# Kernel tuning notes

Hardware: AMD Instinct MI355X
Metric: run time of the kernel (lower is better)

The kernel has to match this reference:

```python
import jax, jax.numpy as jnp
import numpy as np

N = 50000
E = 800000
IN_C = 128
HID = 16
HEADS = 8
OUT_C = 16
NEG_SLOPE = 0.2


def setup_inputs() -> dict:
    key = jax.random.key(0)
    ks = jax.random.split(key, 10)
    s = 1.0 / np.sqrt(IN_C)
    s2 = 1.0 / np.sqrt(HID * HEADS)
    return {
        "x": jax.random.normal(ks[0], (N, IN_C), jnp.float32),
        "edge_index": jax.random.randint(ks[1], (2, E), 0, N, jnp.int64),
        "W1": jax.random.normal(ks[2], (IN_C, HEADS * HID), jnp.float32) * s,
        "a_src1": jax.random.normal(ks[3], (HEADS, HID), jnp.float32) * s,
        "a_dst1": jax.random.normal(ks[4], (HEADS, HID), jnp.float32) * s,
        "b1": jnp.zeros((HEADS * HID,), jnp.float32),
        "W2": jax.random.normal(ks[5], (HEADS * HID, OUT_C), jnp.float32) * s2,
        "a_src2": jax.random.normal(ks[6], (1, OUT_C), jnp.float32) * s2,
        "a_dst2": jax.random.normal(ks[7], (1, OUT_C), jnp.float32) * s2,
        "b2": jnp.zeros((OUT_C,), jnp.float32),
    }


def gat_layer(x, src, dst, W, a_src, a_dst):
    # x: [N, F_in]; W: [F_in, H*C]; a_src/a_dst: [H, C]
    H, C = a_src.shape
    h = (x @ W).reshape(N, H, C)                       # [N, H, C]
    al_s = jnp.einsum('nhc,hc->nh', h, a_src)          # [N, H]
    al_d = jnp.einsum('nhc,hc->nh', h, a_dst)
    e = jax.nn.leaky_relu(al_s[src] + al_d[dst], NEG_SLOPE)  # [E', H]
    # scatter-softmax over incoming edges of each target node
    m = jax.ops.segment_max(e, dst, num_segments=N)    # [N, H]
    w = jnp.exp(e - m[dst])                            # [E', H]
    denom = jax.ops.segment_sum(w, dst, num_segments=N)
    alpha = w / denom[dst]                             # [E', H]
    out = jax.ops.segment_sum(h[src] * alpha[:, :, None], dst, num_segments=N)
    return out                                         # [N, H, C]


def reference(x, edge_index, W1, a_src1, a_dst1, b1, W2, a_src2, a_dst2, b2):
    loops = jnp.arange(N, dtype=edge_index.dtype)
    src = jnp.concatenate([edge_index[0], loops])
    dst = jnp.concatenate([edge_index[1], loops])
    # layer 1: heads=8, concat=True
    h1 = gat_layer(x, src, dst, W1, a_src1, a_dst1).reshape(N, -1) + b1
    h1 = jax.nn.elu(h1)
    # layer 2: heads=1, concat=False (single head -> mean is identity)
    h2 = gat_layer(h1, src, dst, W2, a_src2, a_dst2)[:, 0, :] + b2
    return h2
```

## Files before the change

kernel.cpp:

```cpp
#include <hip/hip_runtime.h>
#include <hip/hip_fp16.h>
#include <math.h>

#define N_NODES 50000
#define NE      800000
#define INC     128
#define F1      128
#define HEADS   8
#define HID     16
#define OUTC    16
#define NEG     0.2f
#define NBKT    196
#define NPART   128
#define N1BLK   ((N_NODES + 63) / 64)

union H4 { ushort4 u; __half h[4]; };
union H8 { uint4 u; __half h[8]; };

typedef _Float16 f16x8 __attribute__((ext_vector_type(8)));
typedef float    f32x4 __attribute__((ext_vector_type(4)));

__global__ __launch_bounds__(256) void prep_kernel(const int* __restrict__ ei,
                                                   int* __restrict__ cnt,
                                                   const float* __restrict__ W1,
                                                   const float* __restrict__ as1,
                                                   const float* __restrict__ ad1,
                                                   __half* __restrict__ W1t,
                                                   __half* __restrict__ waT) {
    __shared__ int h[NBKT];
    int b = blockIdx.x, tid = threadIdx.x;
    if (b < NPART) {
        for (int i = tid; i < NBKT; i += 256) h[i] = 0;
        __syncthreads();
        for (int e = b * 256 + tid; e < NE; e += NPART * 256)
            atomicAdd(&h[ei[NE + e] >> 8], 1);
        __syncthreads();
        for (int i = tid; i < NBKT; i += 256) cnt[i * NPART + b] = h[i];
    } else if (b < NPART + 64) {
        int i = (b - NPART) * 256 + tid;
        int k = i >> 7, nn = i & 127;
        W1t[nn * 128 + k] = __float2half(W1[k * 128 + nn]);
    } else {
        int i = (b - NPART - 64) * 256 + tid;
        int col = i & 15, k = i >> 4;
        int hh = col & 7;
        const float* av = (col < 8) ? as1 : ad1;
        float s = 0.f;
        #pragma unroll
        for (int cc = 0; cc < 16; ++cc)
            s += W1[k * 128 + hh * 16 + cc] * av[hh * 16 + cc];
        waT[col * 128 + k] = __float2half(s);
    }
}

__global__ __launch_bounds__(1024) void scan25k(int* __restrict__ cnt) {
    __shared__ int part[1024];
    const int TOT = NBKT * NPART;
    const int PER = (TOT + 1023) / 1024;
    int tid = threadIdx.x;
    int base = tid * PER;
    int s = 0;
    for (int i = 0; i < PER; ++i) {
        int idx = base + i;
        if (idx < TOT) s += cnt[idx];
    }
    part[tid] = s; __syncthreads();
    for (int off = 1; off < 1024; off <<= 1) {
        int t = (tid >= off) ? part[tid - off] : 0;
        __syncthreads();
        part[tid] += t;
        __syncthreads();
    }
    int run = part[tid] - s;
    for (int i = 0; i < PER; ++i) {
        int idx = base + i;
        if (idx < TOT) { int v = cnt[idx]; cnt[idx] = run; run += v; }
    }
}

__global__ __launch_bounds__(256) void scatter_node1_kernel(
    const int* __restrict__ ei, const int* __restrict__ cnt, int* __restrict__ tmp,
    const float* __restrict__ x, const __half* __restrict__ W1t,
    const __half* __restrict__ waT,
    __half* __restrict__ hfeat, float* __restrict__ als, float* __restrict__ ald)
{
    __shared__ _Float16 Xh[64 * 136];
    __shared__ _Float16 Wt[128 * 136];
    int b = blockIdx.x, tid = threadIdx.x;

    if (b < NPART) {
        int* cur = (int*)Xh;
        for (int i = tid; i < NBKT; i += 256) cur[i] = cnt[i * NPART + b];
        __syncthreads();
        for (int e = b * 256 + tid; e < NE; e += NPART * 256) {
            int s = ei[e], d = ei[NE + e];
            int p = atomicAdd(&cur[d >> 8], 1);
            tmp[p] = s | ((d & 255) << 16);
        }
        return;
    }

    int n0 = (b - NPART) * 64;

    for (int idx = tid; idx < 128 * 16; idx += 256) {
        int row = idx >> 4, c8 = (idx & 15) * 8;
        *(uint4*)(&Wt[row * 136 + c8]) = ((const uint4*)W1t)[idx];
    }
    for (int idx = tid; idx < 64 * 32; idx += 256) {
        int m = idx >> 5, f4 = idx & 31;
        int n = n0 + m;
        float4 v = (n < N_NODES) ? ((const float4*)(x + (size_t)n * INC))[f4]
                                 : make_float4(0.f, 0.f, 0.f, 0.f);
        union { unsigned long long u; _Float16 h[4]; } p;
        p.h[0] = (_Float16)v.x; p.h[1] = (_Float16)v.y;
        p.h[2] = (_Float16)v.z; p.h[3] = (_Float16)v.w;
        *(unsigned long long*)(&Xh[m * 136 + f4 * 4]) = p.u;
    }
    __syncthreads();

    int wave = tid >> 6, lane = tid & 63;
    int colL = lane & 15, q = lane >> 4;
    int nb = wave * 32;

    f32x4 acc[4][2];
    #pragma unroll
    for (int mt = 0; mt < 4; ++mt)
        #pragma unroll
        for (int nt = 0; nt < 2; ++nt)
            acc[mt][nt] = (f32x4){0.f, 0.f, 0.f, 0.f};
    f32x4 acc2 = (f32x4){0.f, 0.f, 0.f, 0.f};

    #pragma unroll
    for (int kb = 0; kb < 4; ++kb) {
        int ko = kb * 32 + q * 8;
        f16x8 b0 = *(const f16x8*)(&Wt[(nb +  0 + colL) * 136 + ko]);
        f16x8 b1 = *(const f16x8*)(&Wt[(nb + 16 + colL) * 136 + ko]);
        #pragma unroll
        for (int mt = 0; mt < 4; ++mt) {
            f16x8 a = *(const f16x8*)(&Xh[(mt * 16 + colL) * 136 + ko]);
            acc[mt][0] = __builtin_amdgcn_mfma_f32_16x16x32_f16(a, b0, acc[mt][0], 0, 0, 0);
            acc[mt][1] = __builtin_amdgcn_mfma_f32_16x16x32_f16(a, b1, acc[mt][1], 0, 0, 0);
        }
        f16x8 bw = *(const f16x8*)(waT + colL * 128 + ko);
        f16x8 aw = *(const f16x8*)(&Xh[(wave * 16 + colL) * 136 + ko]);
        acc2 = __builtin_amdgcn_mfma_f32_16x16x32_f16(aw, bw, acc2, 0, 0, 0);
    }

    #pragma unroll
    for (int nt = 0; nt < 2; ++nt) {
        int col = nb + nt * 16 + colL;
        #pragma unroll
        for (int mt = 0; mt < 4; ++mt) {
            f32x4 d = acc[mt][nt];
            #pragma unroll
            for (int r = 0; r < 4; ++r) {
                int node = n0 + mt * 16 + q * 4 + r;
                if (node < N_NODES) hfeat[(size_t)node * F1 + col] = __float2half(d[r]);
            }
        }
    }
    #pragma unroll
    for (int r = 0; r < 4; ++r) {
        int node = n0 + wave * 16 + q * 4 + r;
        if (node < N_NODES) {
            if (colL < 8) als[node * 8 + colL] = acc2[r];
            else          ald[node * 8 + (colL - 8)] = acc2[r];
        }
    }
}

__global__ __launch_bounds__(256) void bucket_sort(const int* __restrict__ tmp,
                                                   const int* __restrict__ cnt,
                                                   int* __restrict__ rowstart,
                                                   int* __restrict__ csr) {
    __shared__ int h[256];
    int b = blockIdx.x, tid = threadIdx.x;
    int base = cnt[b * NPART];
    int end  = (b == NBKT - 1) ? NE : cnt[(b + 1) * NPART];
    h[tid] = 0; __syncthreads();
    for (int i = base + tid; i < end; i += 256)
        atomicAdd(&h[(tmp[i] >> 16) & 255], 1);
    __syncthreads();
    int v = h[tid];
    for (int off = 1; off < 256; off <<= 1) {
        int t = (tid >= off) ? h[tid - off] : 0;
        __syncthreads();
        h[tid] += t;
        __syncthreads();
    }
    int excl = h[tid] - v;
    int n = (b << 8) + tid;
    if (n <= N_NODES) rowstart[n] = base + excl;
    __syncthreads();
    h[tid] = excl;
    __syncthreads();
    for (int i = base + tid; i < end; i += 256) {
        int e = tmp[i];
        int p = base + atomicAdd(&h[(e >> 16) & 255], 1);
        csr[p] = e & 0xFFFF;
    }
}

__global__ __launch_bounds__(256) void agg1_kernel(
    const int* __restrict__ rowstart, const int* __restrict__ csr,
    const __half* __restrict__ h1, const float* __restrict__ als,
    const float* __restrict__ ald, const float* __restrict__ b1,
    __half* __restrict__ hout)
{
    int tid = threadIdx.x;
    int n = blockIdx.x * 16 + (tid >> 4);
    int lane = tid & 15;
    int c = lane * 8;
    int head = lane >> 1;
    float aldn = ald[n * 8 + head];
    float v0 = als[n * 8 + head] + aldn;
    v0 = fmaxf(v0, NEG * v0);
    float w0 = __expf(v0);
    float sum = w0;
    float a[8];
    {
        H8 hs; hs.u = *(const uint4*)(h1 + (size_t)n * F1 + c);
        #pragma unroll
        for (int i = 0; i < 8; ++i) a[i] = w0 * __half2float(hs.h[i]);
    }
    int r0 = rowstart[n], r1 = rowstart[n + 1];

    float vA = 0.f, vB = 0.f;
    H8 hA, hB; hA.u = make_uint4(0,0,0,0); hB.u = hA.u;
    int sC = 0, sD = 0;
    if (r0 < r1) {
        int s = csr[r0];
        float t = als[s * 8 + head] + aldn;
        vA = fmaxf(t, NEG * t);
        hA.u = *(const uint4*)(h1 + (size_t)s * F1 + c);
    }
    if (r0 + 1 < r1) {
        int s = csr[r0 + 1];
        float t = als[s * 8 + head] + aldn;
        vB = fmaxf(t, NEG * t);
        hB.u = *(const uint4*)(h1 + (size_t)s * F1 + c);
    }
    if (r0 + 2 < r1) sC = csr[r0 + 2];
    if (r0 + 3 < r1) sD = csr[r0 + 3];

    int k = r0;
    for (; k + 1 < r1; k += 2) {
        float vcA = vA, vcB = vB;
        H8 hcA = hA, hcB = hB;
        int sE = (k + 4 < r1) ? csr[k + 4] : 0;
        int sF = (k + 5 < r1) ? csr[k + 5] : 0;
        if (k + 2 < r1) {
            float t = als[sC * 8 + head] + aldn;
            vA = fmaxf(t, NEG * t);
            hA.u = *(const uint4*)(h1 + (size_t)sC * F1 + c);
        }
        if (k + 3 < r1) {
            float t = als[sD * 8 + head] + aldn;
            vB = fmaxf(t, NEG * t);
            hB.u = *(const uint4*)(h1 + (size_t)sD * F1 + c);
        }
        sC = sE; sD = sF;
        float wA = __expf(vcA), wB = __expf(vcB);
        sum += wA + wB;
        #pragma unroll
        for (int i = 0; i < 8; ++i) {
            a[i] = fmaf(wA, __half2float(hcA.h[i]), a[i]);
            a[i] = fmaf(wB, __half2float(hcB.h[i]), a[i]);
        }
    }
    if (k < r1) {
        float wA = __expf(vA);
        sum += wA;
        #pragma unroll
        for (int i = 0; i < 8; ++i) a[i] = fmaf(wA, __half2float(hA.h[i]), a[i]);
    }

    float inv = 1.0f / sum;
    H8 t;
    #pragma unroll
    for (int i = 0; i < 8; ++i) {
        float o = a[i] * inv + b1[c + i];
        o = o > 0.f ? o : (__expf(o) - 1.0f);
        t.h[i] = __float2half(o);
    }
    *(uint4*)(hout + (size_t)n * F1 + c) = t.u;
}

__global__ __launch_bounds__(256) void node2_kernel(
    const __half* __restrict__ h1, const float* __restrict__ W2,
    const float* __restrict__ a_s, const float* __restrict__ a_d,
    __half* __restrict__ h2, float* __restrict__ als2, float* __restrict__ ald2)
{
    __shared__ float W2l[F1 * OUTC];
    for (int i = threadIdx.x; i < F1 * OUTC; i += 256) W2l[i] = W2[i];
    __syncthreads();
    int n = blockIdx.x * blockDim.x + threadIdx.x;
    if (n >= N_NODES) return;

    float o[OUTC];
    #pragma unroll
    for (int c = 0; c < OUTC; ++c) o[c] = 0.f;
    const uint4* xr = (const uint4*)(h1 + (size_t)n * F1);
    for (int k8 = 0; k8 < 16; ++k8) {
        H8 xv; xv.u = xr[k8];
        int k = k8 * 8;
        #pragma unroll
        for (int j = 0; j < 8; ++j) {
            float xf = __half2float(xv.h[j]);
            #pragma unroll
            for (int c = 0; c < OUTC; ++c)
                o[c] = fmaf(xf, W2l[(k + j) * OUTC + c], o[c]);
        }
    }
    H8 s0, s1;
    #pragma unroll
    for (int j = 0; j < 8; ++j) { s0.h[j] = __float2half(o[j]); s1.h[j] = __float2half(o[8 + j]); }
    uint4* h2o = (uint4*)(h2 + (size_t)n * OUTC);
    h2o[0] = s0.u; h2o[1] = s1.u;
    float ps = 0.f, pd = 0.f;
    #pragma unroll
    for (int c = 0; c < OUTC; ++c) { ps += o[c] * a_s[c]; pd += o[c] * a_d[c]; }
    als2[n] = ps; ald2[n] = pd;
}

__global__ __launch_bounds__(256) void agg2_kernel(
    const int* __restrict__ rowstart, const int* __restrict__ csr,
    const __half* __restrict__ h2, const float* __restrict__ als,
    const float* __restrict__ ald, const float* __restrict__ b2,
    float* __restrict__ out)
{
    int tid = threadIdx.x;
    int n = blockIdx.x * 64 + (tid >> 2);
    if (n >= N_NODES) return;
    int c = (tid & 3) * 4;
    float aldn = ald[n];
    float v0 = als[n] + aldn;
    v0 = fmaxf(v0, NEG * v0);
    float w0 = __expf(v0);
    float sum = w0;
    H4 hs; hs.u = *(const ushort4*)(h2 + (size_t)n * OUTC + c);
    float a0 = w0 * __half2float(hs.h[0]), a1 = w0 * __half2float(hs.h[1]);
    float a2 = w0 * __half2float(hs.h[2]), a3 = w0 * __half2float(hs.h[3]);
    int r0 = rowstart[n], r1 = rowstart[n + 1];

    float vA = 0.f, vB = 0.f;
    H4 hA, hB; hA.u = make_ushort4(0,0,0,0); hB.u = hA.u;
    int sC = 0, sD = 0;
    if (r0 < r1) {
        int s = csr[r0];
        float t = als[s] + aldn;
        vA = fmaxf(t, NEG * t);
        hA.u = *(const ushort4*)(h2 + (size_t)s * OUTC + c);
    }
    if (r0 + 1 < r1) {
        int s = csr[r0 + 1];
        float t = als[s] + aldn;
        vB = fmaxf(t, NEG * t);
        hB.u = *(const ushort4*)(h2 + (size_t)s * OUTC + c);
    }
    if (r0 + 2 < r1) sC = csr[r0 + 2];
    if (r0 + 3 < r1) sD = csr[r0 + 3];

    int k = r0;
    for (; k + 1 < r1; k += 2) {
        float vcA = vA, vcB = vB;
        H4 hcA = hA, hcB = hB;
        int sE = (k + 4 < r1) ? csr[k + 4] : 0;
        int sF = (k + 5 < r1) ? csr[k + 5] : 0;
        if (k + 2 < r1) {
            float t = als[sC] + aldn;
            vA = fmaxf(t, NEG * t);
            hA.u = *(const ushort4*)(h2 + (size_t)sC * OUTC + c);
        }
        if (k + 3 < r1) {
            float t = als[sD] + aldn;
            vB = fmaxf(t, NEG * t);
            hB.u = *(const ushort4*)(h2 + (size_t)sD * OUTC + c);
        }
        sC = sE; sD = sF;
        float wA = __expf(vcA), wB = __expf(vcB);
        sum += wA + wB;
        a0 = fmaf(wA, __half2float(hcA.h[0]), a0); a0 = fmaf(wB, __half2float(hcB.h[0]), a0);
        a1 = fmaf(wA, __half2float(hcA.h[1]), a1); a1 = fmaf(wB, __half2float(hcB.h[1]), a1);
        a2 = fmaf(wA, __half2float(hcA.h[2]), a2); a2 = fmaf(wB, __half2float(hcB.h[2]), a2);
        a3 = fmaf(wA, __half2float(hcA.h[3]), a3); a3 = fmaf(wB, __half2float(hcB.h[3]), a3);
    }
    if (k < r1) {
        float wA = __expf(vA);
        sum += wA;
        a0 = fmaf(wA, __half2float(hA.h[0]), a0);
        a1 = fmaf(wA, __half2float(hA.h[1]), a1);
        a2 = fmaf(wA, __half2float(hA.h[2]), a2);
        a3 = fmaf(wA, __half2float(hA.h[3]), a3);
    }

    float inv = 1.0f / sum;
    float4 bv = *(const float4*)(b2 + c);
    float4 o;
    o.x = a0 * inv + bv.x; o.y = a1 * inv + bv.y;
    o.z = a2 * inv + bv.z; o.w = a3 * inv + bv.w;
    *(float4*)(out + (size_t)n * OUTC + c) = o;
}

extern "C" void kernel_launch(void* const* d_in, const int* in_sizes, int n_in,
                              void* d_out, int out_size, void* d_ws, size_t ws_size,
                              hipStream_t stream)
{
    const float* x   = (const float*)d_in[0];
    const int*   ei  = (const int*)  d_in[1];
    const float* W1  = (const float*)d_in[2];
    const float* as1 = (const float*)d_in[3];
    const float* ad1 = (const float*)d_in[4];
    const float* b1  = (const float*)d_in[5];
    const float* W2  = (const float*)d_in[6];
    const float* as2 = (const float*)d_in[7];
    const float* ad2 = (const float*)d_in[8];
    const float* b2  = (const float*)d_in[9];
    float* out = (float*)d_out;

    char* wsb = (char*)d_ws;
    const size_t SZ_H1 = (size_t)N_NODES * F1 * sizeof(__half);
    __half* h1h = (__half*)wsb;
    __half* h1b = (__half*)(wsb + SZ_H1);
    float*  als1 = (float*)(wsb + 2 * SZ_H1);
    float*  ald1 = als1 + (size_t)N_NODES * 8;
    __half* h2f  = (__half*)(ald1 + (size_t)N_NODES * 8);
    float*  als2 = (float*)(h2f + (size_t)N_NODES * OUTC);
    float*  ald2 = als2 + N_NODES;
    __half* w1t  = (__half*)(ald2 + N_NODES);
    __half* waT  = w1t + INC * F1;
    int*    tmp  = (int*)(waT + 16 * INC);
    int*    cnt  = tmp + NE;
    int*    csr  = cnt + NBKT * NPART;
    int*    rowstart = csr + NE;

    prep_kernel <<<NPART + 72, 256, 0, stream>>>(ei, cnt, W1, as1, ad1, w1t, waT);
    scan25k     <<<1, 1024, 0, stream>>>(cnt);
    scatter_node1_kernel<<<NPART + N1BLK, 256, 0, stream>>>(ei, cnt, tmp,
                                                            x, w1t, waT, h1h, als1, ald1);
    bucket_sort <<<NBKT, 256, 0, stream>>>(tmp, cnt, rowstart, csr);

    agg1_kernel<<<N_NODES / 16, 256, 0, stream>>>(rowstart, csr, h1h, als1, ald1, b1, h1b);

    node2_kernel<<<(N_NODES + 255) / 256, 256, 0, stream>>>(h1b, W2, as2, ad2, h2f, als2, ald2);
    agg2_kernel<<<(N_NODES + 63) / 64, 256, 0, stream>>>(rowstart, csr, h2f, als2, ald2, b2, out);
}
```

Measured before the change: 220.3 us.

## Fuse layer-1 aggregation with layer-2 linear projection in one kernel

Merges agg1 and node2 so the ELU-activated layer-1 output is staged in shared memory and immediately multiplied by W2, with attention logits reduced by lane shuffles. This removes the round-trip write and re-read of the N×128 half-precision hidden tensor and one kernel launch. The cost is a W2 load into LDS (8 KB) in every 16-node block (3125 blocks), plus an extra barrier and larger shared footprint, which may reduce occupancy.

```diff
diff --git a/kernel.cpp b/kernel.cpp
--- a/kernel.cpp
+++ b/kernel.cpp
@@ -201,14 +201,22 @@
     }
 }
 
-__global__ __launch_bounds__(256) void agg1_kernel(
+__global__ __launch_bounds__(256) void agg1_node2_kernel(
     const int* __restrict__ rowstart, const int* __restrict__ csr,
     const __half* __restrict__ h1, const float* __restrict__ als,
     const float* __restrict__ ald, const float* __restrict__ b1,
-    __half* __restrict__ hout)
+    const float* __restrict__ W2, const float* __restrict__ a_s2,
+    const float* __restrict__ a_d2,
+    __half* __restrict__ h2, float* __restrict__ als2, float* __restrict__ ald2)
 {
+    __shared__ float    W2l[F1 * OUTC];
+    __shared__ _Float16 hbuf[16][136];
+
     int tid = threadIdx.x;
-    int n = blockIdx.x * 16 + (tid >> 4);
+    for (int i = tid; i < F1 * OUTC; i += 256) W2l[i] = W2[i];
+
+    int nl = tid >> 4;
+    int n = blockIdx.x * 16 + nl;
     int lane = tid & 15;
     int c = lane * 8;
     int head = lane >> 1;
@@ -276,51 +284,35 @@
     }
 
     float inv = 1.0f / sum;
-    H8 t;
+    f16x8 hv;
     #pragma unroll
     for (int i = 0; i < 8; ++i) {
         float o = a[i] * inv + b1[c + i];
         o = o > 0.f ? o : (__expf(o) - 1.0f);
-        t.h[i] = __float2half(o);
-    }
-    *(uint4*)(hout + (size_t)n * F1 + c) = t.u;
-}
-
-__global__ __launch_bounds__(256) void node2_kernel(
-    const __half* __restrict__ h1, const float* __restrict__ W2,
-    const float* __restrict__ a_s, const float* __restrict__ a_d,
-    __half* __restrict__ h2, float* __restrict__ als2, float* __restrict__ ald2)
-{
-    __shared__ float W2l[F1 * OUTC];
-    for (int i = threadIdx.x; i < F1 * OUTC; i += 256) W2l[i] = W2[i];
+        hv[i] = (_Float16)o;
+    }
+    *(f16x8*)(&hbuf[nl][c]) = hv;
     __syncthreads();
-    int n = blockIdx.x * blockDim.x + threadIdx.x;
-    if (n >= N_NODES) return;
-
-    float o[OUTC];
-    #pragma unroll
-    for (int c = 0; c < OUTC; ++c) o[c] = 0.f;
-    const uint4* xr = (const uint4*)(h1 + (size_t)n * F1);
+
+    int c2 = tid & 15;
+    float acc = 0.f;
+    #pragma unroll
     for (int k8 = 0; k8 < 16; ++k8) {
-        H8 xv; xv.u = xr[k8];
-        int k = k8 * 8;
-        #pragma unroll
-        for (int j = 0; j < 8; ++j) {
-            float xf = __half2float(xv.h[j]);
-            #pragma unroll
-            for (int c = 0; c < OUTC; ++c)
-                o[c] = fmaf(xf, W2l[(k + j) * OUTC + c], o[c]);
-        }
-    }
-    H8 s0, s1;
-    #pragma unroll
-    for (int j = 0; j < 8; ++j) { s0.h[j] = __float2half(o[j]); s1.h[j] = __float2half(o[8 + j]); }
-    uint4* h2o = (uint4*)(h2 + (size_t)n * OUTC);
-    h2o[0] = s0.u; h2o[1] = s1.u;
-    float ps = 0.f, pd = 0.f;
-    #pragma unroll
-    for (int c = 0; c < OUTC; ++c) { ps += o[c] * a_s[c]; pd += o[c] * a_d[c]; }
-    als2[n] = ps; ald2[n] = pd;
+        f16x8 xv = *(const f16x8*)(&hbuf[nl][k8 * 8]);
+        #pragma unroll
+        for (int j = 0; j < 8; ++j)
+            acc = fmaf((float)xv[j], W2l[(k8 * 8 + j) * OUTC + c2], acc);
+    }
+    h2[(size_t)n * OUTC + c2] = __float2half(acc);
+
+    float ps = acc * a_s2[c2];
+    float pd = acc * a_d2[c2];
+    #pragma unroll
+    for (int m = 1; m < 16; m <<= 1) {
+        ps += __shfl_xor(ps, m, 64);
+        pd += __shfl_xor(pd, m, 64);
+    }
+    if (c2 == 0) { als2[n] = ps; ald2[n] = pd; }
 }
 
 __global__ __launch_bounds__(256) void agg2_kernel(
@@ -433,6 +425,7 @@
     int*    cnt  = tmp + NE;
     int*    csr  = cnt + NBKT * NPART;
     int*    rowstart = csr + NE;
+    (void)h1b;
 
     prep_kernel <<<NPART + 72, 256, 0, stream>>>(ei, cnt, W1, as1, ad1, w1t, waT);
     scan25k     <<<1, 1024, 0, stream>>>(cnt);
@@ -440,8 +433,8 @@
                                                             x, w1t, waT, h1h, als1, ald1);
     bucket_sort <<<NBKT, 256, 0, stream>>>(tmp, cnt, rowstart, csr);
 
-    agg1_kernel<<<N_NODES / 16, 256, 0, stream>>>(rowstart, csr, h1h, als1, ald1, b1, h1b);
-
-    node2_kernel<<<(N_NODES + 255) / 256, 256, 0, stream>>>(h1b, W2, as2, ad2, h2f, als2, ald2);
+    agg1_node2_kernel<<<N_NODES / 16, 256, 0, stream>>>(rowstart, csr, h1h, als1, ald1, b1,
+                                                        W2, as2, ad2, h2f, als2, ald2);
+
     agg2_kernel<<<(N_NODES + 63) / 64, 256, 0, stream>>>(rowstart, csr, h2f, als2, ald2, b2, out);
 }
```

New measurement: 213.9 us. 2.9% less time.
